# Kernel optimization log

Hardware: AMD Instinct MI355X
Metric: run time of the kernel (lower is better)

## Reference

```python
import jax, jax.numpy as jnp
import numpy as np

N = 100000
E = 1600000
F_IN = 32   # node_features
F_H = 32    # filters
F_OUT = 4


def setup_inputs() -> dict:
    key = jax.random.key(0)
    ks = jax.random.split(key, 24)
    inp = {
        'x': jax.random.normal(ks[0], (N, F_IN), dtype=jnp.float32),
        'edge_index': jax.random.randint(ks[1], (2, E), 0, N, dtype=jnp.int64),
        'edge_weight': jax.random.uniform(ks[2], (E,), dtype=jnp.float32),
        'H': jax.random.normal(ks[3], (N, F_H), dtype=jnp.float32),
    }
    # ChebConv params: W[k] for k in {0,1} (K=2), bias per conv.
    def cheb_params(kw, kb, fin):
        s = 1.0 / np.sqrt(fin)
        W = jax.random.uniform(kw, (2, fin, F_H), jnp.float32, -s, s)
        b = jax.random.uniform(kb, (F_H,), jnp.float32, -s, s)
        return W, b
    names = ['xz', 'hz', 'xr', 'hr', 'xh', 'hh']
    fins = [F_IN, F_H, F_IN, F_H, F_IN, F_H]
    for i, (nm, fin) in enumerate(zip(names, fins)):
        W, b = cheb_params(ks[4 + 2 * i], ks[5 + 2 * i], fin)
        inp['W' + nm] = W
        inp['b' + nm] = b
    s = 1.0 / np.sqrt(F_H)
    inp['lin_w'] = jax.random.uniform(ks[20], (F_H, F_OUT), jnp.float32, -s, s)
    inp['lin_b'] = jax.random.uniform(ks[21], (F_OUT,), jnp.float32, -s, s)
    return inp


def _cheb(x, src, dst, nw, W, b):
    # ChebConv, K=2, sym norm, lambda_max=2 => L_hat = -D^{-1/2} A D^{-1/2}
    # (diagonal of scaled Laplacian cancels exactly: 1 - 1 = 0).
    tx1 = -jax.ops.segment_sum(nw[:, None] * x[src], dst, num_segments=N)
    return x @ W[0] + tx1 @ W[1] + b


def reference(x, edge_index, edge_weight, H,
              Wxz, bxz, Whz, bhz, Wxr, bxr, Whr, bhr, Wxh, bxh, Whh, bhh,
              lin_w, lin_b):
    src, dst = edge_index[0], edge_index[1]
    # remove_self_loops equivalent: zero out self-loop weights
    w = jnp.where(src == dst, 0.0, edge_weight)
    deg = jax.ops.segment_sum(w, src, num_segments=N)
    dinv = jnp.where(deg > 0, jax.lax.rsqrt(jnp.maximum(deg, 1e-30)), 0.0)
    nw = dinv[src] * w * dinv[dst]  # per-edge sym-normalized weight

    Z = jax.nn.sigmoid(_cheb(x, src, dst, nw, Wxz, bxz) +
                       _cheb(H, src, dst, nw, Whz, bhz))
    R = jax.nn.sigmoid(_cheb(x, src, dst, nw, Wxr, bxr) +
                       _cheb(H, src, dst, nw, Whr, bhr))
    H_tilde = jnp.tanh(_cheb(x, src, dst, nw, Wxh, bxh) +
                       _cheb(H * R, src, dst, nw, Whh, bhh))
    h = Z * H + (1.0 - Z) * H_tilde
    out = jax.nn.relu(h) @ lin_w + lin_b
    return (out, h)
```

## Files before the change

kernel.cpp:

```cpp
#include <hip/hip_runtime.h>
#include <hip/hip_bf16.h>
#include <hip/hip_fp16.h>

typedef __hip_bfloat16 bf16;
typedef __attribute__((ext_vector_type(8))) short bf16x8;
typedef __attribute__((ext_vector_type(4))) float f32x4;

#define NN   100000
#define EE   1600000
#define FH   32
#define FOUT 4
#define NBD  782
#define NBS  196
#define CAPB 2432
#define CAPS 8960
#define CAP  64
#define BINBLK 512
#define BINTHR 1024
#define EPB  3125
#define EPT  4
#define MFMA16(a, b, c) __builtin_amdgcn_mfma_f32_16x16x32_bf16(a, b, c, 0, 0, 0)

__device__ __forceinline__ float b2f(bf16 v) { return __bfloat162float(v); }

__device__ __forceinline__ float ldf(const void* p, int i, int f32) {
    return f32 ? ((const float*)p)[i] : b2f(((const bf16*)p)[i]);
}
__device__ __forceinline__ int ldi(const void* p, int i, int i64f) {
    return i64f ? (int)(((const long long*)p)[i]) : ((const int*)p)[i];
}
__device__ __forceinline__ void stf(void* p, int i, int f32, float v) {
    if (f32) ((float*)p)[i] = v;
    else     ((bf16*)p)[i] = __float2bfloat16(v);
}
__device__ __forceinline__ float h2f(unsigned short u) {
    return __half2float(__ushort_as_half(u));
}
__device__ __forceinline__ unsigned short f2h16(float v) {
    return __half_as_ushort(__float2half(v));
}
__device__ __forceinline__ short f2bf(float v) {
    unsigned u = __float_as_uint(v);
    return (short)((u + 0x7FFFu + ((u >> 16) & 1u)) >> 16);
}
__device__ __forceinline__ unsigned q8(float v) {
    int q = (int)rintf(v * 16.f) + 128;
    q = q < 0 ? 0 : (q > 255 ? 255 : q);
    return (unsigned)q;
}
__device__ __forceinline__ float ub(unsigned w, int k) {
    return (float)((w >> (k * 8)) & 0xFFu);
}
__device__ __forceinline__ float4 bfly_g(float4 v) {
    v.x += __shfl_xor(v.x, 8);  v.y += __shfl_xor(v.y, 8);
    v.z += __shfl_xor(v.z, 8);  v.w += __shfl_xor(v.w, 8);
    v.x += __shfl_xor(v.x, 16); v.y += __shfl_xor(v.y, 16);
    v.z += __shfl_xor(v.z, 16); v.w += __shfl_xor(v.w, 16);
    return v;
}
__device__ __forceinline__ bf16x8 bfragT(const short* __restrict__ wt, int idx) {
    return *(const bf16x8*)(wt + idx);
}

__global__ __launch_bounds__(256) void k_prep(
    const void* __restrict__ x, const void* __restrict__ H,
    const void* __restrict__ ei,
    const void* __restrict__ W0, const void* __restrict__ W1,
    const void* __restrict__ W2, const void* __restrict__ W3,
    const void* __restrict__ W4, const void* __restrict__ W5,
    int* __restrict__ flg, int* __restrict__ binCur, int* __restrict__ binCurS,
    short* __restrict__ wt, unsigned* __restrict__ xh,
    unsigned short* __restrict__ xh8) {
    __shared__ int s_fl[2];
    int t = threadIdx.x, b = blockIdx.x;
    if (t == 0) { s_fl[0] = 0; s_fl[1] = 0; }
    __syncthreads();
    {
        float v = b2f(((const bf16*)x)[t]);
        if ((!isfinite(v)) || (fabsf(v) > 100.f)) atomicOr(&s_fl[0], 1);
        int w32 = ((const int*)ei)[t];
        if ((t & 1) && (w32 != 0)) atomicOr(&s_fl[1], 1);
    }
    __syncthreads();
    int f32 = s_fl[0];
    int i64 = s_fl[1] ? 0 : 1;
    if (b == 0 && t == 0) { flg[0] = f32; flg[1] = i64; }
    if (b < 48) {
        int i = b * 256 + t;
        int mat = i >> 11;
        int r = i & 2047;
        int cheb = r >> 10, k = (r >> 5) & 31, n = r & 31;
        const void* W = (mat == 0) ? W0 : (mat == 1) ? W1 : (mat == 2) ? W2
                      : (mat == 3) ? W3 : (mat == 4) ? W4 : W5;
        wt[(((mat << 1) + cheb) << 10) + n * 32 + k] = f2bf(ldf(W, r, f32));
    } else if (b == 48) {
        for (int i = t; i < NBD; i += 256) binCur[i] = i * CAPB;
    } else if (b == 49) {
        for (int i = t; i < NBS; i += 256) binCurS[i] = i * CAPS;
    }
    int i = b * 256 + t;
    if (i < NN * FH) {
        float xv = ldf(x, i, f32);
        float hv = ldf(H, i, f32);
        xh[i] = ((unsigned)f2h16(hv) << 16) | f2h16(xv);
        xh8[i] = (unsigned short)((q8(hv) << 8) | q8(xv));
    }
}

__global__ __launch_bounds__(BINTHR, 8) void k_bin(const void* __restrict__ ei,
                                                   const void* __restrict__ ew,
                                                   const int* __restrict__ flg,
                                                   int* __restrict__ binCur,
                                                   int* __restrict__ binCurS,
                                                   int2* __restrict__ dstRec,
                                                   int* __restrict__ srcRec) {
    __shared__ int hD[NBD], bD[NBD], lofD[NBD];
    __shared__ int hS[NBS], bS[NBS], lofS[NBS];
    __shared__ int sWave[16];
    __shared__ int2 stD[EPB];
    __shared__ int  stS[EPB];
    int t = threadIdx.x;
    int lane = t & 63, wv = t >> 6;
    for (int i = t; i < NBD; i += BINTHR) hD[i] = 0;
    for (int i = t; i < NBS; i += BINTHR) hS[i] = 0;
    __syncthreads();
    int e0 = blockIdx.x * EPB;
    int e1 = e0 + EPB;
    int f32 = flg[0], i64 = flg[1];
    int rs[EPT], rd[EPT], rw[EPT];
    #pragma unroll
    for (int u = 0; u < EPT; u++) {
        int e = e0 + t + u * BINTHR;
        bool v = e < e1;
        int s = v ? ldi(ei, e, i64) : 0;
        int d = v ? ldi(ei, EE + e, i64) : 0;
        float w = (v && s != d) ? ldf(ew, e, f32) : 0.f;
        rs[u] = s; rd[u] = d;
        rw[u] = (int)(f2h16(w) & 0x7FFFu);
        if (v) {
            atomicAdd(&hD[d >> 7], 1);
            atomicAdd(&hS[s >> 9], 1);
        }
    }
    __syncthreads();
    for (int i = t; i < NBD; i += BINTHR)
        bD[i] = (hD[i] > 0) ? atomicAdd(&binCur[i], hD[i]) : 0;
    for (int i = t; i < NBS; i += BINTHR)
        bS[i] = (hS[i] > 0) ? atomicAdd(&binCurS[i], hS[i]) : 0;
    int vD = (t < NBD) ? hD[t] : 0;
    int p = vD;
    #pragma unroll
    for (int ofs = 1; ofs < 64; ofs <<= 1) {
        int u = __shfl_up(p, ofs);
        if (lane >= ofs) p += u;
    }
    if (lane == 63) sWave[wv] = p;
    __syncthreads();
    if (t < 16) {
        int q = sWave[t];
        #pragma unroll
        for (int ofs = 1; ofs < 16; ofs <<= 1) {
            int u = __shfl_up(q, ofs);
            if (t >= ofs) q += u;
        }
        sWave[t] = q;
    }
    __syncthreads();
    if (t < NBD) {
        int incl = p + (wv ? sWave[wv - 1] : 0);
        lofD[t] = incl - vD;
        hD[t] = 0;
    }
    __syncthreads();
    int vS = (t < NBS) ? hS[t] : 0;
    p = vS;
    #pragma unroll
    for (int ofs = 1; ofs < 64; ofs <<= 1) {
        int u = __shfl_up(p, ofs);
        if (lane >= ofs) p += u;
    }
    if (lane == 63) sWave[wv] = p;
    __syncthreads();
    if (t < 16) {
        int q = sWave[t];
        #pragma unroll
        for (int ofs = 1; ofs < 16; ofs <<= 1) {
            int u = __shfl_up(q, ofs);
            if (t >= ofs) q += u;
        }
        sWave[t] = q;
    }
    __syncthreads();
    if (t < NBS) {
        int incl = p + (wv ? sWave[wv - 1] : 0);
        lofS[t] = incl - vS;
        hS[t] = 0;
    }
    __syncthreads();
    #pragma unroll
    for (int u = 0; u < EPT; u++) {
        int e = e0 + t + u * BINTHR;
        if (e < e1) {
            int s = rs[u], d = rd[u], wh = rw[u];
            int bd = d >> 7, bs = s >> 9;
            int rdx = atomicAdd(&hD[bd], 1);
            int rsx = atomicAdd(&hS[bs], 1);
            stD[lofD[bd] + rdx] = make_int2((int)(((unsigned)s << 15) | wh),
                                            (bd << 8) | (d & 127));
            stS[lofS[bs] + rsx] = (int)(((unsigned)bs << 24) |
                                        ((unsigned)(s & 511) << 15) | (unsigned)wh);
        }
    }
    __syncthreads();
    int tot = e1 - e0;
    for (int i = t; i < tot; i += BINTHR) {
        int2 r = stD[i];
        int bin = ((unsigned)r.y) >> 8;
        int g = bD[bin] + (i - lofD[bin]);
        if (g < (bin + 1) * CAPB) dstRec[g] = make_int2(r.x, r.y & 127);
        int u = stS[i];
        int sbin = ((unsigned)u) >> 24;
        int gs = bS[sbin] + (i - lofS[sbin]);
        if (gs < (sbin + 1) * CAPS) srcRec[gs] = u & 0xFFFFFF;
    }
}

__global__ __launch_bounds__(256) void k_degb(const int* __restrict__ binCurS,
                                              const int* __restrict__ srcRec,
                                              float* __restrict__ dinv) {
    __shared__ float lDeg[512];
    int b = blockIdx.x, t = threadIdx.x;
    lDeg[t] = 0.f; lDeg[t + 256] = 0.f;
    __syncthreads();
    int cnt = binCurS[b] - b * CAPS;
    if (cnt > CAPS) cnt = CAPS;
    for (int i = t; i < cnt; i += 256) {
        int r = srcRec[b * CAPS + i];
        atomicAdd(&lDeg[(r >> 15) & 511], h2f((unsigned short)(r & 0x7FFF)));
    }
    __syncthreads();
    #pragma unroll
    for (int k = 0; k < 2; k++) {
        int li = t + k * 256;
        int node = b * 512 + li;
        if (node < NN) {
            float dv = lDeg[li];
            dinv[node] = (dv > 0.f) ? rsqrtf(dv) : 0.f;
        }
    }
}

__global__ __launch_bounds__(256) void k_fillb(const int* __restrict__ binCur,
                                               const int2* __restrict__ dstRec,
                                               const float* __restrict__ dinv,
                                               int* __restrict__ cursor,
                                               int* __restrict__ ell) {
    __shared__ int lCur[128];
    __shared__ int lEll[128 * CAP];
    int b = blockIdx.x, t = threadIdx.x;
    if (t < 128) lCur[t] = 0;
    __syncthreads();
    int cnt = binCur[b] - b * CAPB;
    if (cnt > CAPB) cnt = CAPB;
    for (int i = t; i < cnt; i += 256) {
        int2 r = dstRec[b * CAPB + i];
        int slot = atomicAdd(&lCur[r.y], 1);
        if (slot < CAP) {
            unsigned s = ((unsigned)r.x) >> 15;
            float c = dinv[s] * h2f((unsigned short)(r.x & 0x7FFF));
            lEll[r.y * CAP + slot] = (int)((s << 15) | (f2h16(c) & 0x7FFFu));
        }
    }
    __syncthreads();
    int nodeBase = b * 128;
    for (int i = t; i < 128 * CAP; i += 256) {
        int node = nodeBase + (i >> 6);
        if (node < NN && (i & 63) < lCur[i >> 6])
            ell[(size_t)node * CAP + (i & (CAP - 1))] = lEll[i];
    }
    if (t < 128 && nodeBase + t < NN) {
        int c = lCur[t]; if (c > CAP) c = CAP;
        cursor[nodeBase + t] = c;
    }
}

__global__ __launch_bounds__(256) void k_gather1(const int* __restrict__ cursor,
                                                 const int* __restrict__ ell,
                                                 const float* __restrict__ dinv,
                                                 const unsigned short* __restrict__ xh8,
                                                 unsigned* __restrict__ axah) {
    int t = threadIdx.x;
    int node = blockIdx.x * 8 + (t >> 5);
    if (node >= NN) return;
    int f = t & 31;
    int g = f >> 3, c = f & 7;
    int cnt = cursor[node];
    size_t base = (size_t)node * CAP;
    float4 ax = {0.f, 0.f, 0.f, 0.f}, ah = {0.f, 0.f, 0.f, 0.f};
    float cs = 0.f;
    for (int j = 0; j < cnt; j += 16) {
        int wrd[4]; float cf[4]; uint2 pv[4];
        #pragma unroll
        for (int u = 0; u < 4; u++) {
            int jj = j + u * 4 + g;
            wrd[u] = (jj < cnt) ? ell[base + jj] : 0;
        }
        #pragma unroll
        for (int u = 0; u < 4; u++) {
            int s = ((unsigned)wrd[u]) >> 15;
            cf[u] = h2f((unsigned short)(wrd[u] & 0x7FFF));
            pv[u] = ((const uint2*)xh8)[s * 8 + c];
        }
        #pragma unroll
        for (int u = 0; u < 4; u++) {
            cs += cf[u];
            ax.x += cf[u] * ub(pv[u].x, 0);
            ah.x += cf[u] * ub(pv[u].x, 1);
            ax.y += cf[u] * ub(pv[u].x, 2);
            ah.y += cf[u] * ub(pv[u].x, 3);
            ax.z += cf[u] * ub(pv[u].y, 0);
            ah.z += cf[u] * ub(pv[u].y, 1);
            ax.w += cf[u] * ub(pv[u].y, 2);
            ah.w += cf[u] * ub(pv[u].y, 3);
        }
    }
    ax = bfly_g(ax); ah = bfly_g(ah);
    cs += __shfl_xor(cs, 8);
    cs += __shfl_xor(cs, 16);
    if (g == 0) {
        float dd = -dinv[node];
        float bias = 8.f * cs;
        uint4 o;
        o.x = ((unsigned)f2h16(dd * (ah.x * 0.0625f - bias)) << 16)
            | f2h16(dd * (ax.x * 0.0625f - bias));
        o.y = ((unsigned)f2h16(dd * (ah.y * 0.0625f - bias)) << 16)
            | f2h16(dd * (ax.y * 0.0625f - bias));
        o.z = ((unsigned)f2h16(dd * (ah.z * 0.0625f - bias)) << 16)
            | f2h16(dd * (ax.z * 0.0625f - bias));
        o.w = ((unsigned)f2h16(dd * (ah.w * 0.0625f - bias)) << 16)
            | f2h16(dd * (ax.w * 0.0625f - bias));
        ((uint4*)(axah + (size_t)node * FH))[c] = o;
    }
}

__global__ __launch_bounds__(256) void k_zr_mfma(
    const unsigned* __restrict__ xh, const unsigned* __restrict__ axah,
    const int* __restrict__ flg, const short* __restrict__ wt,
    const void* __restrict__ bxz, const void* __restrict__ bhz,
    const void* __restrict__ bxr, const void* __restrict__ bhr,
    unsigned short* __restrict__ zf16, unsigned short* __restrict__ hr16) {
    int t = threadIdx.x;
    int lane = t & 63, wv = t >> 6;
    int f32 = flg[0];
    int c = lane & 15, quad = lane >> 4, kb = quad * 8;
    int nodeBase = blockIdx.x * 64 + wv * 16;
    int nm = nodeBase + c; if (nm >= NN) nm = NN - 1;

    bf16x8 fx, fHH, fAX, fAH;
    {
        const uint4* p = (const uint4*)(xh + (size_t)nm * FH + kb);
        uint4 a = p[0], b = p[1];
        unsigned wd[8] = {a.x, a.y, a.z, a.w, b.x, b.y, b.z, b.w};
        #pragma unroll
        for (int j = 0; j < 8; j++) {
            fx[j]  = f2bf(h2f((unsigned short)(wd[j] & 0xFFFF)));
            fHH[j] = f2bf(h2f((unsigned short)(wd[j] >> 16)));
        }
    }
    {
        const uint4* p = (const uint4*)(axah + (size_t)nm * FH + kb);
        uint4 a = p[0], b = p[1];
        unsigned wd[8] = {a.x, a.y, a.z, a.w, b.x, b.y, b.z, b.w};
        #pragma unroll
        for (int j = 0; j < 8; j++) {
            fAX[j] = f2bf(h2f((unsigned short)(wd[j] & 0xFFFF)));
            fAH[j] = f2bf(h2f((unsigned short)(wd[j] >> 16)));
        }
    }

    float bz0 = ldf(bxz, c, f32) + ldf(bhz, c, f32);
    float bz1 = ldf(bxz, c + 16, f32) + ldf(bhz, c + 16, f32);
    float br0 = ldf(bxr, c, f32) + ldf(bhr, c, f32);
    float br1 = ldf(bxr, c + 16, f32) + ldf(bhr, c + 16, f32);
    f32x4 az0 = {bz0, bz0, bz0, bz0}, az1 = {bz1, bz1, bz1, bz1};
    f32x4 ar0 = {br0, br0, br0, br0}, ar1 = {br1, br1, br1, br1};

    int i0 = c * 32 + kb;
    int i1 = (c + 16) * 32 + kb;
    az0 = MFMA16(fx,  bfragT(wt, 0 * 1024 + i0), az0);
    az0 = MFMA16(fAX, bfragT(wt, 1 * 1024 + i0), az0);
    az0 = MFMA16(fHH, bfragT(wt, 2 * 1024 + i0), az0);
    az0 = MFMA16(fAH, bfragT(wt, 3 * 1024 + i0), az0);
    az1 = MFMA16(fx,  bfragT(wt, 0 * 1024 + i1), az1);
    az1 = MFMA16(fAX, bfragT(wt, 1 * 1024 + i1), az1);
    az1 = MFMA16(fHH, bfragT(wt, 2 * 1024 + i1), az1);
    az1 = MFMA16(fAH, bfragT(wt, 3 * 1024 + i1), az1);
    ar0 = MFMA16(fx,  bfragT(wt, 4 * 1024 + i0), ar0);
    ar0 = MFMA16(fAX, bfragT(wt, 5 * 1024 + i0), ar0);
    ar0 = MFMA16(fHH, bfragT(wt, 6 * 1024 + i0), ar0);
    ar0 = MFMA16(fAH, bfragT(wt, 7 * 1024 + i0), ar0);
    ar1 = MFMA16(fx,  bfragT(wt, 4 * 1024 + i1), ar1);
    ar1 = MFMA16(fAX, bfragT(wt, 5 * 1024 + i1), ar1);
    ar1 = MFMA16(fHH, bfragT(wt, 6 * 1024 + i1), ar1);
    ar1 = MFMA16(fAH, bfragT(wt, 7 * 1024 + i1), ar1);

    #pragma unroll
    for (int tl = 0; tl < 2; tl++) {
        f32x4 az = tl ? az1 : az0, ar = tl ? ar1 : ar0;
        int f = c + 16 * tl;
        #pragma unroll
        for (int r = 0; r < 4; r++) {
            int node = nodeBase + quad * 4 + r;
            if (node < NN) {
                float zv = 1.f / (1.f + expf(-az[r]));
                float rv = 1.f / (1.f + expf(-ar[r]));
                float Hv = h2f((unsigned short)(xh[(size_t)node * FH + f] >> 16));
                zf16[(size_t)node * FH + f] = f2h16(zv);
                hr16[(size_t)node * FH + f] = f2h16(Hv * rv);
            }
        }
    }
}

__global__ __launch_bounds__(256) void k_gather2(const int* __restrict__ cursor,
                                                 const int* __restrict__ ell,
                                                 const float* __restrict__ dinv,
                                                 const unsigned short* __restrict__ hr16,
                                                 unsigned short* __restrict__ ahr16) {
    int t = threadIdx.x;
    int node = blockIdx.x * 8 + (t >> 5);
    if (node >= NN) return;
    int f = t & 31;
    int g = f >> 3, c = f & 7;
    int cnt = cursor[node];
    size_t base = (size_t)node * CAP;
    float4 acc = {0.f, 0.f, 0.f, 0.f};
    for (int j = 0; j < cnt; j += 16) {
        int wrd[4]; float cf[4]; ushort4 hv[4];
        #pragma unroll
        for (int u = 0; u < 4; u++) {
            int jj = j + u * 4 + g;
            wrd[u] = (jj < cnt) ? ell[base + jj] : 0;
        }
        #pragma unroll
        for (int u = 0; u < 4; u++) {
            int s = ((unsigned)wrd[u]) >> 15;
            cf[u] = h2f((unsigned short)(wrd[u] & 0x7FFF));
            hv[u] = ((const ushort4*)hr16)[s * 8 + c];
        }
        #pragma unroll
        for (int u = 0; u < 4; u++) {
            acc.x += cf[u] * h2f(hv[u].x);
            acc.y += cf[u] * h2f(hv[u].y);
            acc.z += cf[u] * h2f(hv[u].z);
            acc.w += cf[u] * h2f(hv[u].w);
        }
    }
    acc = bfly_g(acc);
    if (g == 0) {
        float dd = -dinv[node];
        ushort4 o = {f2h16(dd * acc.x), f2h16(dd * acc.y),
                     f2h16(dd * acc.z), f2h16(dd * acc.w)};
        ((ushort4*)(ahr16 + (size_t)node * FH))[c] = o;
    }
}

__global__ __launch_bounds__(256) void k_final(
    const unsigned* __restrict__ xh, const unsigned* __restrict__ axah,
    const int* __restrict__ flg, const short* __restrict__ wt,
    const unsigned short* __restrict__ zf16,
    const unsigned short* __restrict__ hr16,
    const unsigned short* __restrict__ ahr16,
    const void* __restrict__ bxh, const void* __restrict__ bhh,
    const void* __restrict__ lin_w, const void* __restrict__ lin_b,
    void* __restrict__ out) {
    __shared__ float srh[64][FH + 1];
    __shared__ float slw[FH * FOUT];
    __shared__ float slb[FOUT];

    int t = threadIdx.x;
    int lane = t & 63, wv = t >> 6;
    int f32 = flg[0];
    int c = lane & 15, quad = lane >> 4, kb = quad * 8;
    int nodeBase = blockIdx.x * 64 + wv * 16;
    int nm = nodeBase + c; if (nm >= NN) nm = NN - 1;

    if (t < FH * FOUT) slw[t] = ldf(lin_w, t, f32);
    if (t < FOUT) slb[t] = ldf(lin_b, t, f32);

    bf16x8 fx, fAX, fHR, fAHR;
    {
        const uint4* p = (const uint4*)(xh + (size_t)nm * FH + kb);
        uint4 a = p[0], b = p[1];
        unsigned wd[8] = {a.x, a.y, a.z, a.w, b.x, b.y, b.z, b.w};
        #pragma unroll
        for (int j = 0; j < 8; j++)
            fx[j] = f2bf(h2f((unsigned short)(wd[j] & 0xFFFF)));
    }
    {
        const uint4* p = (const uint4*)(axah + (size_t)nm * FH + kb);
        uint4 a = p[0], b = p[1];
        unsigned wd[8] = {a.x, a.y, a.z, a.w, b.x, b.y, b.z, b.w};
        #pragma unroll
        for (int j = 0; j < 8; j++)
            fAX[j] = f2bf(h2f((unsigned short)(wd[j] & 0xFFFF)));
    }
    {
        const uint4* p = (const uint4*)(hr16 + (size_t)nm * FH + kb);
        uint4 a = p[0];
        unsigned wd[4] = {a.x, a.y, a.z, a.w};
        #pragma unroll
        for (int j = 0; j < 8; j++)
            fHR[j] = f2bf(h2f((unsigned short)((wd[j >> 1] >> ((j & 1) * 16)) & 0xFFFF)));
    }
    {
        const uint4* p = (const uint4*)(ahr16 + (size_t)nm * FH + kb);
        uint4 a = p[0];
        unsigned wd[4] = {a.x, a.y, a.z, a.w};
        #pragma unroll
        for (int j = 0; j < 8; j++)
            fAHR[j] = f2bf(h2f((unsigned short)((wd[j >> 1] >> ((j & 1) * 16)) & 0xFFFF)));
    }

    float bh0 = ldf(bxh, c, f32) + ldf(bhh, c, f32);
    float bh1 = ldf(bxh, c + 16, f32) + ldf(bhh, c + 16, f32);
    f32x4 a0 = {bh0, bh0, bh0, bh0}, a1 = {bh1, bh1, bh1, bh1};

    int i0 = c * 32 + kb;
    int i1 = (c + 16) * 32 + kb;
    a0 = MFMA16(fx,   bfragT(wt,  8 * 1024 + i0), a0);
    a0 = MFMA16(fAX,  bfragT(wt,  9 * 1024 + i0), a0);
    a0 = MFMA16(fHR,  bfragT(wt, 10 * 1024 + i0), a0);
    a0 = MFMA16(fAHR, bfragT(wt, 11 * 1024 + i0), a0);
    a1 = MFMA16(fx,   bfragT(wt,  8 * 1024 + i1), a1);
    a1 = MFMA16(fAX,  bfragT(wt,  9 * 1024 + i1), a1);
    a1 = MFMA16(fHR,  bfragT(wt, 10 * 1024 + i1), a1);
    a1 = MFMA16(fAHR, bfragT(wt, 11 * 1024 + i1), a1);

    #pragma unroll
    for (int tl = 0; tl < 2; tl++) {
        f32x4 a = tl ? a1 : a0;
        int f = c + 16 * tl;
        #pragma unroll
        for (int r = 0; r < 4; r++) {
            int node = nodeBase + quad * 4 + r;
            if (node < NN) {
                float ht = tanhf(a[r]);
                float zv = h2f(zf16[(size_t)node * FH + f]);
                float Hv = h2f((unsigned short)(xh[(size_t)node * FH + f] >> 16));
                float hval = zv * Hv + (1.f - zv) * ht;
                stf(out, NN * FOUT + node * FH + f, f32, hval);
                srh[wv * 16 + quad * 4 + r][f] = hval > 0.f ? hval : 0.f;
            }
        }
    }
    __syncthreads();

    int nl = t >> 2, fo = t & 3;
    int node2 = blockIdx.x * 64 + nl;
    if (node2 < NN) {
        float acc = slb[fo];
        #pragma unroll
        for (int k = 0; k < FH; k++) acc += srh[nl][k] * slw[k * FOUT + fo];
        stf(out, node2 * FOUT + fo, f32, acc);
    }
}

extern "C" void kernel_launch(void* const* d_in, const int* in_sizes, int n_in,
                              void* d_out, int out_size, void* d_ws, size_t ws_size,
                              hipStream_t stream) {
    const void* x   = d_in[0];
    const void* ei  = d_in[1];
    const void* ew  = d_in[2];
    const void* H   = d_in[3];
    const void* Wxz = d_in[4];
    const void* bxz = d_in[5];
    const void* Whz = d_in[6];
    const void* bhz = d_in[7];
    const void* Wxr = d_in[8];
    const void* bxr = d_in[9];
    const void* Whr = d_in[10];
    const void* bhr = d_in[11];
    const void* Wxh = d_in[12];
    const void* bxh = d_in[13];
    const void* Whh = d_in[14];
    const void* bhh = d_in[15];
    const void* lnw = d_in[16];
    const void* lnb = d_in[17];

    char* base = (char*)d_ws;
    int*            flg     = (int*)base;            base += 64;
    int*            binCur  = (int*)base;            base += (NBD * 4 + 63) & ~63;
    int*            binCurS = (int*)base;            base += (NBS * 4 + 63) & ~63;
    float*          dinv    = (float*)base;          base += (size_t)NN * 4;
    int*            cursor  = (int*)base;            base += (size_t)NN * 4;
    short*          wt      = (short*)base;          base += (12288 * 2 + 63) & ~63;
    unsigned*       xh      = (unsigned*)base;       base += (size_t)NN * FH * 4;
    unsigned short* xh8     = (unsigned short*)base; base += (size_t)NN * FH * 2;
    unsigned*       axah    = (unsigned*)base;       base += (size_t)NN * FH * 4;
    unsigned short* zf16    = (unsigned short*)base; base += (size_t)NN * FH * 2;
    unsigned short* hr16    = (unsigned short*)base; base += (size_t)NN * FH * 2;
    unsigned short* ahr16   = (unsigned short*)base; base += (size_t)NN * FH * 2;
    int*            ell     = (int*)base;            base += (size_t)NN * CAP * 4;
    int2*           dstRec  = (int2*)base;           base += (size_t)NBD * CAPB * 8;
    int*            srcRec  = (int*)base;

    const int pb   = (NN * FH + 255) / 256;
    const int n8b  = (NN + 7) / 8;
    const int n64b = (NN + 63) / 64;

    k_prep<<<pb, 256, 0, stream>>>(x, H, ei, Wxz, Whz, Wxr, Whr, Wxh, Whh,
                                   flg, binCur, binCurS, wt, xh, xh8);
    k_bin<<<BINBLK, BINTHR, 0, stream>>>(ei, ew, flg, binCur, binCurS,
                                         dstRec, srcRec);
    k_degb<<<NBS, 256, 0, stream>>>(binCurS, srcRec, dinv);
    k_fillb<<<NBD, 256, 0, stream>>>(binCur, dstRec, dinv, cursor, ell);
    k_gather1<<<n8b, 256, 0, stream>>>(cursor, ell, dinv, xh8, axah);
    k_zr_mfma<<<n64b, 256, 0, stream>>>(xh, axah, flg, wt,
                                        bxz, bhz, bxr, bhr, zf16, hr16);
    k_gather2<<<n8b, 256, 0, stream>>>(cursor, ell, dinv, hr16, ahr16);
    k_final<<<n64b, 256, 0, stream>>>(xh, axah, flg, wt, zf16, hr16, ahr16,
                                      bxh, bhh, lnw, lnb, d_out);
}
```

Baseline: 257.4 us.

## Move Z gate computation into final kernel and split dst records into SoA

```diff
diff --git a/kernel.cpp b/kernel.cpp
--- a/kernel.cpp
+++ b/kernel.cpp
@@ -112,7 +112,8 @@
                                                    const int* __restrict__ flg,
                                                    int* __restrict__ binCur,
                                                    int* __restrict__ binCurS,
-                                                   int2* __restrict__ dstRec,
+                                                   int* __restrict__ dstRecA,
+                                                   unsigned char* __restrict__ dstRecB,
                                                    int* __restrict__ srcRec) {
     __shared__ int hD[NBD], bD[NBD], lofD[NBD];
     __shared__ int hS[NBS], bS[NBS], lofS[NBS];
@@ -217,7 +218,10 @@
         int2 r = stD[i];
         int bin = ((unsigned)r.y) >> 8;
         int g = bD[bin] + (i - lofD[bin]);
-        if (g < (bin + 1) * CAPB) dstRec[g] = make_int2(r.x, r.y & 127);
+        if (g < (bin + 1) * CAPB) {
+            dstRecA[g] = r.x;
+            dstRecB[g] = (unsigned char)(r.y & 127);
+        }
         int u = stS[i];
         int sbin = ((unsigned)u) >> 24;
         int gs = bS[sbin] + (i - lofS[sbin]);
@@ -251,7 +255,8 @@
 }
 
 __global__ __launch_bounds__(256) void k_fillb(const int* __restrict__ binCur,
-                                               const int2* __restrict__ dstRec,
+                                               const int* __restrict__ dstRecA,
+                                               const unsigned char* __restrict__ dstRecB,
                                                const float* __restrict__ dinv,
                                                int* __restrict__ cursor,
                                                int* __restrict__ ell) {
@@ -263,12 +268,13 @@
     int cnt = binCur[b] - b * CAPB;
     if (cnt > CAPB) cnt = CAPB;
     for (int i = t; i < cnt; i += 256) {
-        int2 r = dstRec[b * CAPB + i];
-        int slot = atomicAdd(&lCur[r.y], 1);
+        int ra = dstRecA[b * CAPB + i];
+        int d7 = dstRecB[b * CAPB + i];
+        int slot = atomicAdd(&lCur[d7], 1);
         if (slot < CAP) {
-            unsigned s = ((unsigned)r.x) >> 15;
-            float c = dinv[s] * h2f((unsigned short)(r.x & 0x7FFF));
-            lEll[r.y * CAP + slot] = (int)((s << 15) | (f2h16(c) & 0x7FFFu));
+            unsigned s = ((unsigned)ra) >> 15;
+            float c = dinv[s] * h2f((unsigned short)(ra & 0x7FFF));
+            lEll[d7 * CAP + slot] = (int)((s << 15) | (f2h16(c) & 0x7FFFu));
         }
     }
     __syncthreads();
@@ -284,11 +290,11 @@
     }
 }
 
-__global__ __launch_bounds__(256) void k_gather1(const int* __restrict__ cursor,
-                                                 const int* __restrict__ ell,
-                                                 const float* __restrict__ dinv,
-                                                 const unsigned short* __restrict__ xh8,
-                                                 unsigned* __restrict__ axah) {
+__global__ __launch_bounds__(256, 8) void k_gather1(const int* __restrict__ cursor,
+                                                    const int* __restrict__ ell,
+                                                    const float* __restrict__ dinv,
+                                                    const unsigned short* __restrict__ xh8,
+                                                    unsigned* __restrict__ axah) {
     int t = threadIdx.x;
     int node = blockIdx.x * 8 + (t >> 5);
     if (node >= NN) return;
@@ -343,12 +349,11 @@
     }
 }
 
-__global__ __launch_bounds__(256) void k_zr_mfma(
+__global__ __launch_bounds__(256) void k_r_mfma(
     const unsigned* __restrict__ xh, const unsigned* __restrict__ axah,
     const int* __restrict__ flg, const short* __restrict__ wt,
-    const void* __restrict__ bxz, const void* __restrict__ bhz,
     const void* __restrict__ bxr, const void* __restrict__ bhr,
-    unsigned short* __restrict__ zf16, unsigned short* __restrict__ hr16) {
+    unsigned short* __restrict__ hr16) {
     int t = threadIdx.x;
     int lane = t & 63, wv = t >> 6;
     int f32 = flg[0];
@@ -378,23 +383,12 @@
         }
     }
 
-    float bz0 = ldf(bxz, c, f32) + ldf(bhz, c, f32);
-    float bz1 = ldf(bxz, c + 16, f32) + ldf(bhz, c + 16, f32);
     float br0 = ldf(bxr, c, f32) + ldf(bhr, c, f32);
     float br1 = ldf(bxr, c + 16, f32) + ldf(bhr, c + 16, f32);
-    f32x4 az0 = {bz0, bz0, bz0, bz0}, az1 = {bz1, bz1, bz1, bz1};
     f32x4 ar0 = {br0, br0, br0, br0}, ar1 = {br1, br1, br1, br1};
 
     int i0 = c * 32 + kb;
     int i1 = (c + 16) * 32 + kb;
-    az0 = MFMA16(fx,  bfragT(wt, 0 * 1024 + i0), az0);
-    az0 = MFMA16(fAX, bfragT(wt, 1 * 1024 + i0), az0);
-    az0 = MFMA16(fHH, bfragT(wt, 2 * 1024 + i0), az0);
-    az0 = MFMA16(fAH, bfragT(wt, 3 * 1024 + i0), az0);
-    az1 = MFMA16(fx,  bfragT(wt, 0 * 1024 + i1), az1);
-    az1 = MFMA16(fAX, bfragT(wt, 1 * 1024 + i1), az1);
-    az1 = MFMA16(fHH, bfragT(wt, 2 * 1024 + i1), az1);
-    az1 = MFMA16(fAH, bfragT(wt, 3 * 1024 + i1), az1);
     ar0 = MFMA16(fx,  bfragT(wt, 4 * 1024 + i0), ar0);
     ar0 = MFMA16(fAX, bfragT(wt, 5 * 1024 + i0), ar0);
     ar0 = MFMA16(fHH, bfragT(wt, 6 * 1024 + i0), ar0);
@@ -406,27 +400,25 @@
 
     #pragma unroll
     for (int tl = 0; tl < 2; tl++) {
-        f32x4 az = tl ? az1 : az0, ar = tl ? ar1 : ar0;
+        f32x4 ar = tl ? ar1 : ar0;
         int f = c + 16 * tl;
         #pragma unroll
         for (int r = 0; r < 4; r++) {
             int node = nodeBase + quad * 4 + r;
             if (node < NN) {
-                float zv = 1.f / (1.f + expf(-az[r]));
                 float rv = 1.f / (1.f + expf(-ar[r]));
                 float Hv = h2f((unsigned short)(xh[(size_t)node * FH + f] >> 16));
-                zf16[(size_t)node * FH + f] = f2h16(zv);
                 hr16[(size_t)node * FH + f] = f2h16(Hv * rv);
             }
         }
     }
 }
 
-__global__ __launch_bounds__(256) void k_gather2(const int* __restrict__ cursor,
-                                                 const int* __restrict__ ell,
-                                                 const float* __restrict__ dinv,
-                                                 const unsigned short* __restrict__ hr16,
-                                                 unsigned short* __restrict__ ahr16) {
+__global__ __launch_bounds__(256, 8) void k_gather2(const int* __restrict__ cursor,
+                                                    const int* __restrict__ ell,
+                                                    const float* __restrict__ dinv,
+                                                    const unsigned short* __restrict__ hr16,
+                                                    unsigned short* __restrict__ ahr16) {
     int t = threadIdx.x;
     int node = blockIdx.x * 8 + (t >> 5);
     if (node >= NN) return;
@@ -468,9 +460,9 @@
 __global__ __launch_bounds__(256) void k_final(
     const unsigned* __restrict__ xh, const unsigned* __restrict__ axah,
     const int* __restrict__ flg, const short* __restrict__ wt,
-    const unsigned short* __restrict__ zf16,
     const unsigned short* __restrict__ hr16,
     const unsigned short* __restrict__ ahr16,
+    const void* __restrict__ bxz, const void* __restrict__ bhz,
     const void* __restrict__ bxh, const void* __restrict__ bhh,
     const void* __restrict__ lin_w, const void* __restrict__ lin_b,
     void* __restrict__ out) {
@@ -488,22 +480,26 @@
     if (t < FH * FOUT) slw[t] = ldf(lin_w, t, f32);
     if (t < FOUT) slb[t] = ldf(lin_b, t, f32);
 
-    bf16x8 fx, fAX, fHR, fAHR;
+    bf16x8 fx, fHH, fAX, fAH, fHR, fAHR;
     {
         const uint4* p = (const uint4*)(xh + (size_t)nm * FH + kb);
         uint4 a = p[0], b = p[1];
         unsigned wd[8] = {a.x, a.y, a.z, a.w, b.x, b.y, b.z, b.w};
         #pragma unroll
-        for (int j = 0; j < 8; j++)
-            fx[j] = f2bf(h2f((unsigned short)(wd[j] & 0xFFFF)));
+        for (int j = 0; j < 8; j++) {
+            fx[j]  = f2bf(h2f((unsigned short)(wd[j] & 0xFFFF)));
+            fHH[j] = f2bf(h2f((unsigned short)(wd[j] >> 16)));
+        }
     }
     {
         const uint4* p = (const uint4*)(axah + (size_t)nm * FH + kb);
         uint4 a = p[0], b = p[1];
         unsigned wd[8] = {a.x, a.y, a.z, a.w, b.x, b.y, b.z, b.w};
         #pragma unroll
-        for (int j = 0; j < 8; j++)
+        for (int j = 0; j < 8; j++) {
             fAX[j] = f2bf(h2f((unsigned short)(wd[j] & 0xFFFF)));
+            fAH[j] = f2bf(h2f((unsigned short)(wd[j] >> 16)));
+        }
     }
     {
         const uint4* p = (const uint4*)(hr16 + (size_t)nm * FH + kb);
@@ -522,12 +518,23 @@
             fAHR[j] = f2bf(h2f((unsigned short)((wd[j >> 1] >> ((j & 1) * 16)) & 0xFFFF)));
     }
 
+    float bz0 = ldf(bxz, c, f32) + ldf(bhz, c, f32);
+    float bz1 = ldf(bxz, c + 16, f32) + ldf(bhz, c + 16, f32);
     float bh0 = ldf(bxh, c, f32) + ldf(bhh, c, f32);
     float bh1 = ldf(bxh, c + 16, f32) + ldf(bhh, c + 16, f32);
+    f32x4 az0 = {bz0, bz0, bz0, bz0}, az1 = {bz1, bz1, bz1, bz1};
     f32x4 a0 = {bh0, bh0, bh0, bh0}, a1 = {bh1, bh1, bh1, bh1};
 
     int i0 = c * 32 + kb;
     int i1 = (c + 16) * 32 + kb;
+    az0 = MFMA16(fx,   bfragT(wt,  0 * 1024 + i0), az0);
+    az0 = MFMA16(fAX,  bfragT(wt,  1 * 1024 + i0), az0);
+    az0 = MFMA16(fHH,  bfragT(wt,  2 * 1024 + i0), az0);
+    az0 = MFMA16(fAH,  bfragT(wt,  3 * 1024 + i0), az0);
+    az1 = MFMA16(fx,   bfragT(wt,  0 * 1024 + i1), az1);
+    az1 = MFMA16(fAX,  bfragT(wt,  1 * 1024 + i1), az1);
+    az1 = MFMA16(fHH,  bfragT(wt,  2 * 1024 + i1), az1);
+    az1 = MFMA16(fAH,  bfragT(wt,  3 * 1024 + i1), az1);
     a0 = MFMA16(fx,   bfragT(wt,  8 * 1024 + i0), a0);
     a0 = MFMA16(fAX,  bfragT(wt,  9 * 1024 + i0), a0);
     a0 = MFMA16(fHR,  bfragT(wt, 10 * 1024 + i0), a0);
@@ -540,13 +547,14 @@
     #pragma unroll
     for (int tl = 0; tl < 2; tl++) {
         f32x4 a = tl ? a1 : a0;
+        f32x4 az = tl ? az1 : az0;
         int f = c + 16 * tl;
         #pragma unroll
         for (int r = 0; r < 4; r++) {
             int node = nodeBase + quad * 4 + r;
             if (node < NN) {
                 float ht = tanhf(a[r]);
-                float zv = h2f(zf16[(size_t)node * FH + f]);
+                float zv = 1.f / (1.f + expf(-az[r]));
                 float Hv = h2f((unsigned short)(xh[(size_t)node * FH + f] >> 16));
                 float hval = zv * Hv + (1.f - zv) * ht;
                 stf(out, NN * FOUT + node * FH + f, f32, hval);
@@ -598,11 +606,11 @@
     unsigned*       xh      = (unsigned*)base;       base += (size_t)NN * FH * 4;
     unsigned short* xh8     = (unsigned short*)base; base += (size_t)NN * FH * 2;
     unsigned*       axah    = (unsigned*)base;       base += (size_t)NN * FH * 4;
-    unsigned short* zf16    = (unsigned short*)base; base += (size_t)NN * FH * 2;
     unsigned short* hr16    = (unsigned short*)base; base += (size_t)NN * FH * 2;
     unsigned short* ahr16   = (unsigned short*)base; base += (size_t)NN * FH * 2;
     int*            ell     = (int*)base;            base += (size_t)NN * CAP * 4;
-    int2*           dstRec  = (int2*)base;           base += (size_t)NBD * CAPB * 8;
+    int*            dstRecA = (int*)base;            base += (size_t)NBD * CAPB * 4;
+    unsigned char*  dstRecB = (unsigned char*)base;  base += ((size_t)NBD * CAPB + 63) & ~(size_t)63;
     int*            srcRec  = (int*)base;
 
     const int pb   = (NN * FH + 255) / 256;
@@ -612,13 +620,13 @@
     k_prep<<<pb, 256, 0, stream>>>(x, H, ei, Wxz, Whz, Wxr, Whr, Wxh, Whh,
                                    flg, binCur, binCurS, wt, xh, xh8);
     k_bin<<<BINBLK, BINTHR, 0, stream>>>(ei, ew, flg, binCur, binCurS,
-                                         dstRec, srcRec);
+                                         dstRecA, dstRecB, srcRec);
     k_degb<<<NBS, 256, 0, stream>>>(binCurS, srcRec, dinv);
-    k_fillb<<<NBD, 256, 0, stream>>>(binCur, dstRec, dinv, cursor, ell);
+    k_fillb<<<NBD, 256, 0, stream>>>(binCur, dstRecA, dstRecB, dinv,
+                                     cursor, ell);
     k_gather1<<<n8b, 256, 0, stream>>>(cursor, ell, dinv, xh8, axah);
-    k_zr_mfma<<<n64b, 256, 0, stream>>>(xh, axah, flg, wt,
-                                        bxz, bhz, bxr, bhr, zf16, hr16);
+    k_r_mfma<<<n64b, 256, 0, stream>>>(xh, axah, flg, wt, bxr, bhr, hr16);
     k_gather2<<<n8b, 256, 0, stream>>>(cursor, ell, dinv, hr16, ahr16);
-    k_final<<<n64b, 256, 0, stream>>>(xh, axah, flg, wt, zf16, hr16, ahr16,
-                                      bxh, bhh, lnw, lnb, d_out);
-}
+    k_final<<<n64b, 256, 0, stream>>>(xh, axah, flg, wt, hr16, ahr16,
+                                      bxz, bhz, bxh, bhh, lnw, lnb, d_out);
+}
```

New measurement: 259.2 us. Within noise of the previous version (+0.7%).
